# Kernel optimization log

Hardware: AMD Instinct MI355X
Metric: run time of the kernel (lower is better)

The kernel has to match this reference:

```python
import jax, jax.numpy as jnp
import numpy as np

N_NODES = 100000
N_EDGES = 1200000
D = 64            # in_channels == hidden_channels
N_GRAPHS = 512
N_CLASSES = 10
N_LAYERS = 3
BN_EPS = 1e-5


def setup_inputs() -> dict:
    key = jax.random.key(0)
    ks = jax.random.split(key, 16)
    x = jax.random.normal(ks[0], (N_NODES, D), dtype=jnp.float32)
    edge_index = jax.random.randint(ks[1], (2, N_EDGES), 0, N_NODES, dtype=jnp.int64)
    batch = jnp.sort(jax.random.randint(ks[2], (N_NODES,), 0, N_GRAPHS, dtype=jnp.int64))
    s = 1.0 / np.sqrt(D)
    # all GIN layers share shape since in_channels == hidden_channels
    mlp_w1 = jax.random.uniform(ks[3], (N_LAYERS, D, D), jnp.float32, -s, s)
    mlp_b1 = jax.random.uniform(ks[4], (N_LAYERS, D), jnp.float32, -s, s)
    mlp_w2 = jax.random.uniform(ks[5], (N_LAYERS, D, D), jnp.float32, -s, s)
    mlp_b2 = jax.random.uniform(ks[6], (N_LAYERS, D), jnp.float32, -s, s)
    bn_g = jnp.ones((N_LAYERS, D), jnp.float32)
    bn_b = jnp.zeros((N_LAYERS, D), jnp.float32)
    hw1 = jax.random.uniform(ks[7], (D, D), jnp.float32, -s, s)
    hb1 = jax.random.uniform(ks[8], (D,), jnp.float32, -s, s)
    hg1 = jnp.ones((D,), jnp.float32)
    hbb1 = jnp.zeros((D,), jnp.float32)
    hw2 = jax.random.uniform(ks[9], (D, D // 2), jnp.float32, -s, s)
    hb2 = jax.random.uniform(ks[10], (D // 2,), jnp.float32, -s, s)
    hg2 = jnp.ones((D // 2,), jnp.float32)
    hbb2 = jnp.zeros((D // 2,), jnp.float32)
    s2 = 1.0 / np.sqrt(D // 2)
    ow = jax.random.uniform(ks[11], (D // 2, N_CLASSES), jnp.float32, -s2, s2)
    ob = jax.random.uniform(ks[12], (N_CLASSES,), jnp.float32, -s2, s2)
    return dict(x=x, edge_index=edge_index, batch=batch,
                mlp_w1=mlp_w1, mlp_b1=mlp_b1, mlp_w2=mlp_w2, mlp_b2=mlp_b2,
                bn_g=bn_g, bn_b=bn_b,
                hw1=hw1, hb1=hb1, hg1=hg1, hbb1=hbb1,
                hw2=hw2, hb2=hb2, hg2=hg2, hbb2=hbb2, ow=ow, ob=ob)


def _bn(x, g, b):
    # training-mode BatchNorm1d: biased variance over the batch (node/graph) dim
    mu = jnp.mean(x, axis=0)
    var = jnp.mean((x - mu) ** 2, axis=0)
    return g * (x - mu) * jax.lax.rsqrt(var + BN_EPS) + b


def reference(x, edge_index, batch, mlp_w1, mlp_b1, mlp_w2, mlp_b2, bn_g, bn_b,
              hw1, hb1, hg1, hbb1, hw2, hb2, hg2, hbb2, ow, ob):
    src, dst = edge_index[0], edge_index[1]
    h = x
    for l in range(N_LAYERS):
        # GINConv (eps=0): h_i <- MLP(h_i + sum_{j in N(i)} h_j)
        agg = jax.ops.segment_sum(h[src], dst, num_segments=N_NODES)
        z = h + agg
        z = jax.nn.relu(z @ mlp_w1[l] + mlp_b1[l]) @ mlp_w2[l] + mlp_b2[l]
        h = jax.nn.relu(_bn(z, bn_g[l], bn_b[l]))
        # dropout omitted (deterministic eval)
    # global mean pool per graph
    sums = jax.ops.segment_sum(h, batch, num_segments=N_GRAPHS)
    cnts = jax.ops.segment_sum(jnp.ones((N_NODES,), h.dtype), batch, num_segments=N_GRAPHS)
    g = sums / jnp.maximum(cnts, 1.0)[:, None]
    g = jax.nn.relu(_bn(g @ hw1 + hb1, hg1, hbb1))
    g = jax.nn.relu(_bn(g @ hw2 + hb2, hg2, hbb2))
    return g @ ow + ob
```

## Files before the change

### kernel.cpp

```cpp
#include <hip/hip_runtime.h>
#include <hip/hip_bf16.h>

#define N_NODES 100000
#define N_EDGES 1200000
#define NG 512

typedef float f32;
typedef unsigned short u16;
typedef unsigned short us8 __attribute__((ext_vector_type(8)));
typedef __bf16 bf16x8 __attribute__((ext_vector_type(8)));
typedef float f32x16 __attribute__((ext_vector_type(16)));

__device__ __forceinline__ f32 bf2f(u16 v) {
  return __uint_as_float(((unsigned)v) << 16);
}
__device__ __forceinline__ u16 f2bf(f32 f) {
  __hip_bfloat16 b = __float2bfloat16(f);
  return *reinterpret_cast<u16*>(&b);
}

__global__ void k_detect(const int* __restrict__ w, int* __restrict__ flag) {
  int t = threadIdx.x;
  int acc = 0;
  #pragma unroll
  for (int k = 0; k < 8; ++k) acc |= w[(t * 8 + k) * 2 + 1];
  if (acc) atomicOr(flag, 1);
}

__global__ void k_count(const int* __restrict__ w, const int* __restrict__ flag,
                        int* __restrict__ deg, int* __restrict__ rank) {
  int e = blockIdx.x * 256 + threadIdx.x;
  if (e >= N_EDGES) return;
  int d = flag[0] ? w[N_EDGES + e] : w[2 * (N_EDGES + e)];
  rank[e] = atomicAdd(&deg[d], 1);
}

__global__ void k_scan1(const int* __restrict__ deg, int* __restrict__ incl, int* __restrict__ bsums) {
  __shared__ int sd[256];
  int t = threadIdx.x, b = blockIdx.x;
  int base = b * 1024 + t * 4;
  int v0 = (base + 0 < N_NODES) ? deg[base + 0] : 0;
  int v1 = (base + 1 < N_NODES) ? deg[base + 1] : 0;
  int v2 = (base + 2 < N_NODES) ? deg[base + 2] : 0;
  int v3 = (base + 3 < N_NODES) ? deg[base + 3] : 0;
  int s = v0 + v1 + v2 + v3;
  sd[t] = s; __syncthreads();
  for (int off = 1; off < 256; off <<= 1) {
    int x = (t >= off) ? sd[t - off] : 0; __syncthreads();
    sd[t] += x; __syncthreads();
  }
  int run = sd[t] - s;
  run += v0; if (base + 0 < N_NODES) incl[base + 0] = run;
  run += v1; if (base + 1 < N_NODES) incl[base + 1] = run;
  run += v2; if (base + 2 < N_NODES) incl[base + 2] = run;
  run += v3; if (base + 3 < N_NODES) incl[base + 3] = run;
  if (t == 255) bsums[b] = sd[255];
}

__global__ void k_scan2(int* __restrict__ bsums, int nb) {
  __shared__ int sd[128];
  int t = threadIdx.x;
  int v = (t < nb) ? bsums[t] : 0;
  sd[t] = v; __syncthreads();
  for (int off = 1; off < 128; off <<= 1) {
    int x = (t >= off) ? sd[t - off] : 0; __syncthreads();
    sd[t] += x; __syncthreads();
  }
  if (t < nb) bsums[t] = sd[t] - v;
}

__global__ void k_scan3(const int* __restrict__ incl, const int* __restrict__ bsums,
                        int* __restrict__ offs) {
  int i = blockIdx.x * 256 + threadIdx.x;
  if (i >= N_NODES) return;
  int start = (i == 0) ? 0 : (incl[i - 1] + bsums[(i - 1) >> 10]);
  offs[i] = start;
  if (i == N_NODES - 1) offs[N_NODES] = incl[i] + bsums[i >> 10];
}

__global__ void k_fill(const int* __restrict__ w, const int* __restrict__ flag,
                       const int* __restrict__ offs, const int* __restrict__ rank,
                       int* __restrict__ csr) {
  int e = blockIdx.x * 256 + threadIdx.x;
  if (e >= N_EDGES) return;
  int is32 = flag[0];
  int s = is32 ? w[e] : w[2 * e];
  int d = is32 ? w[N_EDGES + e] : w[2 * (N_EDGES + e)];
  csr[offs[d] + rank[e]] = s;
}

__global__ void k_cast(const f32* __restrict__ x, u16* __restrict__ h) {
  int i = blockIdx.x * 256 + threadIdx.x;
  if (i >= N_NODES * 8) return;
  float4 v0 = ((const float4*)x)[i * 2 + 0];
  float4 v1 = ((const float4*)x)[i * 2 + 1];
  us8 r;
  r[0] = f2bf(v0.x); r[1] = f2bf(v0.y); r[2] = f2bf(v0.z); r[3] = f2bf(v0.w);
  r[4] = f2bf(v1.x); r[5] = f2bf(v1.y); r[6] = f2bf(v1.z); r[7] = f2bf(v1.w);
  *(us8*)&h[i * 8] = r;
}

__global__ __launch_bounds__(256) void k_agg(const u16* __restrict__ hin,
                                             u16* __restrict__ z,
                                             const int* __restrict__ offs,
                                             const int* __restrict__ csr) {
  int wid = blockIdx.x * 4 + (threadIdx.x >> 6);
  int lane = threadIdx.x & 63;
  int slot = lane >> 3;
  int fl = (lane & 7) << 3;
  int e0 = offs[wid], e1 = offs[wid + 1];
  f32 a0[8] = {0,0,0,0,0,0,0,0};
  f32 a1[8] = {0,0,0,0,0,0,0,0};
  int e = e0 + slot;
  for (; e + 8 < e1; e += 16) {
    int s0 = csr[e], s1 = csr[e + 8];
    us8 v0 = *(const us8*)&hin[s0 * 64 + fl];
    us8 v1 = *(const us8*)&hin[s1 * 64 + fl];
    #pragma unroll
    for (int k = 0; k < 8; ++k) { a0[k] += bf2f(v0[k]); a1[k] += bf2f(v1[k]); }
  }
  if (e < e1) {
    us8 v0 = *(const us8*)&hin[csr[e] * 64 + fl];
    #pragma unroll
    for (int k = 0; k < 8; ++k) a0[k] += bf2f(v0[k]);
  }
  #pragma unroll
  for (int k = 0; k < 8; ++k) a0[k] += a1[k];
  #pragma unroll
  for (int k = 0; k < 8; ++k) {
    a0[k] += __shfl_xor(a0[k], 8);
    a0[k] += __shfl_xor(a0[k], 16);
    a0[k] += __shfl_xor(a0[k], 32);
  }
  if (slot == 0) {
    us8 sv = *(const us8*)&hin[wid * 64 + fl];
    us8 o;
    #pragma unroll
    for (int k = 0; k < 8; ++k) o[k] = f2bf(a0[k] + bf2f(sv[k]));
    *(us8*)&z[wid * 64 + fl] = o;
  }
}

__global__ __launch_bounds__(256) void k_mlp(
    const u16* __restrict__ zin, f32* __restrict__ yout,
    const f32* __restrict__ W1, const f32* __restrict__ b1,
    const f32* __restrict__ W2, const f32* __restrict__ b2,
    f32* __restrict__ stsum, f32* __restrict__ stsq)
{
  __shared__ __align__(16) u16 zs[128 * 64];
  __shared__ __align__(16) u16 wt1[64 * 64];
  __shared__ __align__(16) u16 wt2[64 * 64];
  __shared__ __align__(16) u16 mid[4 * 32 * 64];
  __shared__ f32 b1s[64], b2s[64], blks[64], blkq[64];
  const int t = threadIdx.x;
  char* zb = (char*)zs; char* w1b = (char*)wt1; char* w2b = (char*)wt2; char* mb = (char*)mid;
  const int base = blockIdx.x * 128;
  #pragma unroll
  for (int r = 0; r < 4; ++r) {
    int off = r * 4096 + t * 16;
    int row = off >> 7, c = off & 127;
    *(us8*)(zb + row * 128 + (c ^ ((row & 7) << 4))) =
        *(const us8*)((const char*)(zin + (size_t)base * 64) + off);
  }
  #pragma unroll
  for (int i0 = 0; i0 < 16; ++i0) {
    int i = i0 * 256 + t;
    int k = i >> 6, c = i & 63;
    int off = c * 128 + ((k * 2) ^ ((c & 7) << 4));
    *(u16*)(w1b + off) = f2bf(W1[i]);
    *(u16*)(w2b + off) = f2bf(W2[i]);
  }
  if (t < 64) { b1s[t] = b1[t]; b2s[t] = b2[t]; blks[t] = 0.f; blkq[t] = 0.f; }
  __syncthreads();
  const int wv = t >> 6, l = t & 63;
  const int lr = l & 31, lh = l >> 5;
  f32x16 acc0, acc1;
  #pragma unroll
  for (int i = 0; i < 16; ++i) { acc0[i] = 0.f; acc1[i] = 0.f; }
  #pragma unroll
  for (int s = 0; s < 4; ++s) {
    int kb = s * 32 + lh * 16;
    int arow = wv * 32 + lr;
    bf16x8 a  = *(bf16x8*)(zb + arow * 128 + (kb ^ ((arow & 7) << 4)));
    bf16x8 bA = *(bf16x8*)(w1b + lr * 128 + (kb ^ ((lr & 7) << 4)));
    bf16x8 bB = *(bf16x8*)(w1b + (lr + 32) * 128 + (kb ^ (((lr + 32) & 7) << 4)));
    acc0 = __builtin_amdgcn_mfma_f32_32x32x16_bf16(a, bA, acc0, 0, 0, 0);
    acc1 = __builtin_amdgcn_mfma_f32_32x32x16_bf16(a, bB, acc1, 0, 0, 0);
  }
  #pragma unroll
  for (int g = 0; g < 16; ++g) {
    int rowl = (g & 3) + 8 * (g >> 2) + 4 * lh;
    int roff = wv * 4096 + rowl * 128;
    int sw = (rowl & 7) << 4;
    *(u16*)(mb + roff + ((lr * 2) ^ sw))        = f2bf(fmaxf(acc0[g] + b1s[lr], 0.f));
    *(u16*)(mb + roff + (((lr + 32) * 2) ^ sw)) = f2bf(fmaxf(acc1[g] + b1s[lr + 32], 0.f));
  }
  asm volatile("s_waitcnt lgkmcnt(0)" ::: "memory");
  #pragma unroll
  for (int i = 0; i < 16; ++i) { acc0[i] = 0.f; acc1[i] = 0.f; }
  #pragma unroll
  for (int s = 0; s < 4; ++s) {
    int kb = s * 32 + lh * 16;
    bf16x8 a  = *(bf16x8*)(mb + wv * 4096 + lr * 128 + (kb ^ ((lr & 7) << 4)));
    bf16x8 bA = *(bf16x8*)(w2b + lr * 128 + (kb ^ ((lr & 7) << 4)));
    bf16x8 bB = *(bf16x8*)(w2b + (lr + 32) * 128 + (kb ^ (((lr + 32) & 7) << 4)));
    acc0 = __builtin_amdgcn_mfma_f32_32x32x16_bf16(a, bA, acc0, 0, 0, 0);
    acc1 = __builtin_amdgcn_mfma_f32_32x32x16_bf16(a, bB, acc1, 0, 0, 0);
  }
  f32 ps0 = 0, pq0 = 0, ps1 = 0, pq1 = 0;
  #pragma unroll
  for (int g = 0; g < 16; ++g) {
    int rowl = (g & 3) + 8 * (g >> 2) + 4 * lh;
    int node = base + wv * 32 + rowl;
    if (node < N_NODES) {
      f32 y0 = acc0[g] + b2s[lr];
      f32 y1 = acc1[g] + b2s[lr + 32];
      yout[(size_t)node * 64 + lr] = y0;
      yout[(size_t)node * 64 + lr + 32] = y1;
      ps0 += y0; pq0 += y0 * y0;
      ps1 += y1; pq1 += y1 * y1;
    }
  }
  atomicAdd(&blks[lr], ps0);      atomicAdd(&blkq[lr], pq0);
  atomicAdd(&blks[lr + 32], ps1); atomicAdd(&blkq[lr + 32], pq1);
  __syncthreads();
  if (t < 64) { atomicAdd(&stsum[t], blks[t]); atomicAdd(&stsq[t], blkq[t]); }
}

__global__ void k_hfin(const f32* __restrict__ st, const f32* __restrict__ g,
                       const f32* __restrict__ b, f32* __restrict__ ss, f32 invn, int d) {
  int t = threadIdx.x;
  if (t < d) {
    f32 m = st[t] * invn;
    f32 var = st[64 + t] * invn - m * m;
    f32 inv = rsqrtf(var + 1e-5f);
    f32 sc = g[t] * inv;
    ss[t] = sc;
    ss[64 + t] = b[t] - m * sc;
  }
}

__global__ void k_bnapply(const f32* __restrict__ y, u16* __restrict__ h,
                          const f32* __restrict__ ss) {
  int i = blockIdx.x * 256 + threadIdx.x;
  if (i >= N_NODES * 8) return;
  int c0 = (i & 7) * 8;
  float4 v0 = ((const float4*)y)[i * 2 + 0];
  float4 v1 = ((const float4*)y)[i * 2 + 1];
  us8 r;
  r[0] = f2bf(fmaxf(fmaf(v0.x, ss[c0 + 0], ss[64 + c0 + 0]), 0.f));
  r[1] = f2bf(fmaxf(fmaf(v0.y, ss[c0 + 1], ss[64 + c0 + 1]), 0.f));
  r[2] = f2bf(fmaxf(fmaf(v0.z, ss[c0 + 2], ss[64 + c0 + 2]), 0.f));
  r[3] = f2bf(fmaxf(fmaf(v0.w, ss[c0 + 3], ss[64 + c0 + 3]), 0.f));
  r[4] = f2bf(fmaxf(fmaf(v1.x, ss[c0 + 4], ss[64 + c0 + 4]), 0.f));
  r[5] = f2bf(fmaxf(fmaf(v1.y, ss[c0 + 5], ss[64 + c0 + 5]), 0.f));
  r[6] = f2bf(fmaxf(fmaf(v1.z, ss[c0 + 6], ss[64 + c0 + 6]), 0.f));
  r[7] = f2bf(fmaxf(fmaf(v1.w, ss[c0 + 7], ss[64 + c0 + 7]), 0.f));
  *(us8*)&h[i * 8] = r;
}

__global__ void k_pool(const u16* __restrict__ h, const int* __restrict__ bw,
                       const int* __restrict__ flag,
                       f32* __restrict__ gsum, f32* __restrict__ gcnt) {
  int wid = (blockIdx.x * blockDim.x + threadIdx.x) >> 6;
  int lane = threadIdx.x & 63;
  const int nw = (256 * 256) >> 6;
  const int per = (N_NODES + nw - 1) / nw;
  int s = wid * per; int e = s + per; if (e > N_NODES) e = N_NODES;
  if (s >= e) return;
  int is32 = flag[0];
  int g = is32 ? bw[s] : bw[2 * s];
  f32 acc = 0.f, cnt = 0.f;
  for (int i = s; i < e; ++i) {
    int gi = is32 ? bw[i] : bw[2 * i];
    if (gi != g) {
      atomicAdd(&gsum[g * 64 + lane], acc);
      if (lane == 0) atomicAdd(&gcnt[g], cnt);
      g = gi; acc = 0.f; cnt = 0.f;
    }
    acc += bf2f(h[i * 64 + lane]);
    cnt += 1.f;
  }
  atomicAdd(&gsum[g * 64 + lane], acc);
  if (lane == 0) atomicAdd(&gcnt[g], cnt);
}

__global__ __launch_bounds__(256) void k_head1(const f32* __restrict__ gsum, const f32* __restrict__ gcnt,
                                               const f32* __restrict__ W, const f32* __restrict__ bias,
                                               f32* __restrict__ p, f32* __restrict__ st) {
  __shared__ f32 Ws[4096];
  __shared__ f32 zs[4][64];
  __shared__ f32 bs[64], bq[64];
  int t = threadIdx.x;
  for (int i = t; i < 4096; i += 256) Ws[i] = W[i];
  if (t < 64) { bs[t] = 0.f; bq[t] = 0.f; }
  int wave = t >> 6, lane = t & 63;
  int row = blockIdx.x * 4 + wave;
  f32 z = gsum[row * 64 + lane] / fmaxf(gcnt[row], 1.f);
  zs[wave][lane] = z;
  __syncthreads();
  f32 y = bias[lane];
  for (int f = 0; f < 64; ++f) y = fmaf(zs[wave][f], Ws[f * 64 + lane], y);
  p[row * 64 + lane] = y;
  atomicAdd(&bs[lane], y);
  atomicAdd(&bq[lane], y * y);
  __syncthreads();
  if (t < 64) { atomicAdd(&st[t], bs[t]); atomicAdd(&st[64 + t], bq[t]); }
}

__global__ __launch_bounds__(256) void k_head2(const f32* __restrict__ p1, const f32* __restrict__ ss,
                                               const f32* __restrict__ W, const f32* __restrict__ bias,
                                               f32* __restrict__ p2, f32* __restrict__ st) {
  __shared__ f32 Ws[2048];
  __shared__ f32 zs[4][64];
  __shared__ f32 bs[32], bq[32];
  int t = threadIdx.x;
  for (int i = t; i < 2048; i += 256) Ws[i] = W[i];
  if (t < 32) { bs[t] = 0.f; bq[t] = 0.f; }
  int wave = t >> 6, lane = t & 63;
  int row = blockIdx.x * 4 + wave;
  f32 z = fmaxf(fmaf(p1[row * 64 + lane], ss[lane], ss[64 + lane]), 0.f);
  zs[wave][lane] = z;
  __syncthreads();
  if (lane < 32) {
    f32 y = bias[lane];
    for (int f = 0; f < 64; ++f) y = fmaf(zs[wave][f], Ws[f * 32 + lane], y);
    p2[row * 32 + lane] = y;
    atomicAdd(&bs[lane], y);
    atomicAdd(&bq[lane], y * y);
  }
  __syncthreads();
  if (t < 32) { atomicAdd(&st[t], bs[t]); atomicAdd(&st[64 + t], bq[t]); }
}

__global__ __launch_bounds__(256) void k_head3(const f32* __restrict__ p2, const f32* __restrict__ ss,
                                               const f32* __restrict__ W, const f32* __restrict__ bias,
                                               f32* __restrict__ out) {
  __shared__ f32 Ws[320];
  __shared__ f32 obs[10];
  __shared__ f32 zs[4][32];
  int t = threadIdx.x;
  for (int i = t; i < 320; i += 256) Ws[i] = W[i];
  if (t < 10) obs[t] = bias[t];
  int wave = t >> 6, lane = t & 63;
  int row = blockIdx.x * 4 + wave;
  if (lane < 32) zs[wave][lane] = fmaxf(fmaf(p2[row * 32 + lane], ss[lane], ss[64 + lane]), 0.f);
  __syncthreads();
  if (lane < 10) {
    f32 o = obs[lane];
    for (int f = 0; f < 32; ++f) o = fmaf(zs[wave][f], Ws[f * 10 + lane], o);
    out[row * 10 + lane] = o;
  }
}

extern "C" void kernel_launch(void* const* d_in, const int* in_sizes, int n_in,
                              void* d_out, int out_size, void* d_ws, size_t ws_size,
                              hipStream_t stream) {
  (void)in_sizes; (void)n_in; (void)out_size; (void)ws_size;
  const f32* x    = (const f32*)d_in[0];
  const int* eiw  = (const int*)d_in[1];
  const int* btw  = (const int*)d_in[2];
  const f32* mw1  = (const f32*)d_in[3];
  const f32* mb1  = (const f32*)d_in[4];
  const f32* mw2  = (const f32*)d_in[5];
  const f32* mb2  = (const f32*)d_in[6];
  const f32* bng  = (const f32*)d_in[7];
  const f32* bnb  = (const f32*)d_in[8];
  const f32* hw1  = (const f32*)d_in[9];
  const f32* hb1  = (const f32*)d_in[10];
  const f32* hg1  = (const f32*)d_in[11];
  const f32* hbb1 = (const f32*)d_in[12];
  const f32* hw2  = (const f32*)d_in[13];
  const f32* hb2  = (const f32*)d_in[14];
  const f32* hg2  = (const f32*)d_in[15];
  const f32* hbb2 = (const f32*)d_in[16];
  const f32* ow   = (const f32*)d_in[17];
  const f32* ob   = (const f32*)d_in[18];
  f32* out = (f32*)d_out;

  int* deg    = (int*)d_ws;
  int* incl   = deg + N_NODES;
  int* bsums  = incl + N_NODES;
  int* flag   = bsums + 128;
  int* offs   = flag + 4;
  int* rank   = offs + 100004;
  int* csr    = rank + N_EDGES;
  u16* hbuf   = (u16*)(csr + N_EDGES);
  u16* zbuf   = hbuf + (size_t)N_NODES * 64;
  f32* ybuf   = (f32*)(zbuf + (size_t)100096 * 64);
  f32* stats  = ybuf + (size_t)N_NODES * 64;
  f32* ss     = stats + 1024;
  f32* ss2    = ss + 128;
  f32* gsum   = ss2 + 128;
  f32* gcnt   = gsum + NG * 64;
  f32* p1     = gcnt + NG;
  f32* p2     = p1 + NG * 64;

  hipMemsetAsync(deg, 0, N_NODES * sizeof(int), stream);
  hipMemsetAsync(flag, 0, sizeof(int), stream);
  hipMemsetAsync(stats, 0, 1024 * sizeof(f32), stream);
  hipMemsetAsync(gsum, 0, (NG * 64 + NG) * sizeof(f32), stream);

  k_detect<<<1, 256, 0, stream>>>(eiw, flag);
  k_count<<<(N_EDGES + 255) / 256, 256, 0, stream>>>(eiw, flag, deg, rank);
  k_scan1<<<(N_NODES + 1023) / 1024, 256, 0, stream>>>(deg, incl, bsums);
  k_scan2<<<1, 128, 0, stream>>>(bsums, (N_NODES + 1023) / 1024);
  k_scan3<<<(N_NODES + 255) / 256, 256, 0, stream>>>(incl, bsums, offs);
  k_fill<<<(N_EDGES + 255) / 256, 256, 0, stream>>>(eiw, flag, offs, rank, csr);

  const int AGG_GRID = N_NODES / 4;
  const int MLP_GRID = (N_NODES + 127) / 128;
  const int C8_GRID  = (N_NODES * 8 + 255) / 256;

  k_cast<<<C8_GRID, 256, 0, stream>>>(x, hbuf);
  k_agg<<<AGG_GRID, 256, 0, stream>>>(hbuf, zbuf, offs, csr);
  k_mlp<<<MLP_GRID, 256, 0, stream>>>(zbuf, ybuf, mw1,        mb1,       mw2,        mb2,       stats + 0,   stats + 64);
  k_hfin<<<1, 64, 0, stream>>>(stats + 0, bng + 0, bnb + 0, ss, 1.f / N_NODES, 64);
  k_bnapply<<<C8_GRID, 256, 0, stream>>>(ybuf, hbuf, ss);
  k_agg<<<AGG_GRID, 256, 0, stream>>>(hbuf, zbuf, offs, csr);
  k_mlp<<<MLP_GRID, 256, 0, stream>>>(zbuf, ybuf, mw1 + 4096, mb1 + 64,  mw2 + 4096, mb2 + 64,  stats + 128, stats + 192);
  k_hfin<<<1, 64, 0, stream>>>(stats + 128, bng + 64, bnb + 64, ss, 1.f / N_NODES, 64);
  k_bnapply<<<C8_GRID, 256, 0, stream>>>(ybuf, hbuf, ss);
  k_agg<<<AGG_GRID, 256, 0, stream>>>(hbuf, zbuf, offs, csr);
  k_mlp<<<MLP_GRID, 256, 0, stream>>>(zbuf, ybuf, mw1 + 8192, mb1 + 128, mw2 + 8192, mb2 + 128, stats + 256, stats + 320);
  k_hfin<<<1, 64, 0, stream>>>(stats + 256, bng + 128, bnb + 128, ss, 1.f / N_NODES, 64);
  k_bnapply<<<C8_GRID, 256, 0, stream>>>(ybuf, hbuf, ss);

  k_pool<<<256, 256, 0, stream>>>(hbuf, btw, flag, gsum, gcnt);
  k_head1<<<NG / 4, 256, 0, stream>>>(gsum, gcnt, hw1, hb1, p1, stats + 384);
  k_hfin<<<1, 64, 0, stream>>>(stats + 384, hg1, hbb1, ss, 1.f / NG, 64);
  k_head2<<<NG / 4, 256, 0, stream>>>(p1, ss, hw2, hb2, p2, stats + 512);
  k_hfin<<<1, 64, 0, stream>>>(stats + 512, hg2, hbb2, ss2, 1.f / NG, 32);
  k_head3<<<NG / 4, 256, 0, stream>>>(p2, ss2, ow, ob, out);
}
```

Before: 521.8 us.

## Fuse BN finalize into consumers, stage MLP output via LDS, vectorize CSR build

Removes the separate k_hfin launches by computing BatchNorm scale/shift inside each consumer kernel. The last layer's BN apply is folded into the pooling kernel, which now reads the fp32 pre-BN output directly. The MLP epilogue stages results through LDS so global stores become coalesced float4 writes. Count and fill process two edges per thread with vector loads, and the four memsets are merged into one. Every block now recomputes the stats, and pooling reads fp32 instead of bf16 data.

```diff
diff --git a/kernel.cpp b/kernel.cpp
--- a/kernel.cpp
+++ b/kernel.cpp
@@ -29,10 +29,20 @@
 
 __global__ void k_count(const int* __restrict__ w, const int* __restrict__ flag,
                         int* __restrict__ deg, int* __restrict__ rank) {
-  int e = blockIdx.x * 256 + threadIdx.x;
-  if (e >= N_EDGES) return;
-  int d = flag[0] ? w[N_EDGES + e] : w[2 * (N_EDGES + e)];
-  rank[e] = atomicAdd(&deg[d], 1);
+  int e2 = blockIdx.x * 256 + threadIdx.x;
+  if (e2 >= N_EDGES / 2) return;
+  int d0, d1;
+  if (flag[0]) {
+    int2 dd = *(const int2*)&w[N_EDGES + 2 * e2];
+    d0 = dd.x; d1 = dd.y;
+  } else {
+    int4 dd = *(const int4*)&w[2 * N_EDGES + 4 * e2];
+    d0 = dd.x; d1 = dd.z;
+  }
+  int2 rk;
+  rk.x = atomicAdd(&deg[d0], 1);
+  rk.y = atomicAdd(&deg[d1], 1);
+  *(int2*)&rank[2 * e2] = rk;
 }
 
 __global__ void k_scan1(const int* __restrict__ deg, int* __restrict__ incl, int* __restrict__ bsums) {
@@ -81,12 +91,21 @@
 __global__ void k_fill(const int* __restrict__ w, const int* __restrict__ flag,
                        const int* __restrict__ offs, const int* __restrict__ rank,
                        int* __restrict__ csr) {
-  int e = blockIdx.x * 256 + threadIdx.x;
-  if (e >= N_EDGES) return;
-  int is32 = flag[0];
-  int s = is32 ? w[e] : w[2 * e];
-  int d = is32 ? w[N_EDGES + e] : w[2 * (N_EDGES + e)];
-  csr[offs[d] + rank[e]] = s;
+  int e2 = blockIdx.x * 256 + threadIdx.x;
+  if (e2 >= N_EDGES / 2) return;
+  int s0, s1, d0, d1;
+  if (flag[0]) {
+    int2 sv = *(const int2*)&w[2 * e2];
+    int2 dv = *(const int2*)&w[N_EDGES + 2 * e2];
+    s0 = sv.x; s1 = sv.y; d0 = dv.x; d1 = dv.y;
+  } else {
+    int4 sv = *(const int4*)&w[4 * e2];
+    int4 dv = *(const int4*)&w[2 * N_EDGES + 4 * e2];
+    s0 = sv.x; s1 = sv.z; d0 = dv.x; d1 = dv.z;
+  }
+  int2 rk = *(const int2*)&rank[2 * e2];
+  csr[offs[d0] + rk.x] = s0;
+  csr[offs[d1] + rk.y] = s1;
 }
 
 __global__ void k_cast(const f32* __restrict__ x, u16* __restrict__ h) {
@@ -147,13 +166,16 @@
     const f32* __restrict__ W2, const f32* __restrict__ b2,
     f32* __restrict__ stsum, f32* __restrict__ stsq)
 {
-  __shared__ __align__(16) u16 zs[128 * 64];
-  __shared__ __align__(16) u16 wt1[64 * 64];
-  __shared__ __align__(16) u16 wt2[64 * 64];
-  __shared__ __align__(16) u16 mid[4 * 32 * 64];
-  __shared__ f32 b1s[64], b2s[64], blks[64], blkq[64];
+  __shared__ __align__(16) char lds[50176];
+  char* zb  = lds;
+  char* w1b = lds + 16384;
+  char* w2b = lds + 24576;
+  char* mb  = lds + 32768;
+  f32* b1s  = (f32*)(lds + 49152);
+  f32* b2s  = b1s + 64;
+  f32* blks = b2s + 64;
+  f32* blkq = blks + 64;
   const int t = threadIdx.x;
-  char* zb = (char*)zs; char* w1b = (char*)wt1; char* w2b = (char*)wt2; char* mb = (char*)mid;
   const int base = blockIdx.x * 128;
   #pragma unroll
   for (int r = 0; r < 4; ++r) {
@@ -207,42 +229,50 @@
     acc0 = __builtin_amdgcn_mfma_f32_32x32x16_bf16(a, bA, acc0, 0, 0, 0);
     acc1 = __builtin_amdgcn_mfma_f32_32x32x16_bf16(a, bB, acc1, 0, 0, 0);
   }
+  __syncthreads();
+  char* yb = lds + wv * 8192;
   f32 ps0 = 0, pq0 = 0, ps1 = 0, pq1 = 0;
   #pragma unroll
   for (int g = 0; g < 16; ++g) {
     int rowl = (g & 3) + 8 * (g >> 2) + 4 * lh;
-    int node = base + wv * 32 + rowl;
-    if (node < N_NODES) {
-      f32 y0 = acc0[g] + b2s[lr];
-      f32 y1 = acc1[g] + b2s[lr + 32];
-      yout[(size_t)node * 64 + lr] = y0;
-      yout[(size_t)node * 64 + lr + 32] = y1;
+    f32 y0 = acc0[g] + b2s[lr];
+    f32 y1 = acc1[g] + b2s[lr + 32];
+    *(f32*)(yb + rowl * 256 + lr * 4)        = y0;
+    *(f32*)(yb + rowl * 256 + (lr + 32) * 4) = y1;
+    if (base + wv * 32 + rowl < N_NODES) {
       ps0 += y0; pq0 += y0 * y0;
       ps1 += y1; pq1 += y1 * y1;
     }
   }
+  asm volatile("s_waitcnt lgkmcnt(0)" ::: "memory");
+  __builtin_amdgcn_sched_barrier(0);
+  #pragma unroll
+  for (int k = 0; k < 8; ++k) {
+    int row = k * 4 + (l >> 4);
+    float4 v = *(float4*)(yb + row * 256 + (l & 15) * 16);
+    int node = base + wv * 32 + row;
+    if (node < N_NODES)
+      *(float4*)&yout[(size_t)node * 64 + (l & 15) * 4] = v;
+  }
   atomicAdd(&blks[lr], ps0);      atomicAdd(&blkq[lr], pq0);
   atomicAdd(&blks[lr + 32], ps1); atomicAdd(&blkq[lr + 32], pq1);
   __syncthreads();
   if (t < 64) { atomicAdd(&stsum[t], blks[t]); atomicAdd(&stsq[t], blkq[t]); }
 }
 
-__global__ void k_hfin(const f32* __restrict__ st, const f32* __restrict__ g,
-                       const f32* __restrict__ b, f32* __restrict__ ss, f32 invn, int d) {
-  int t = threadIdx.x;
-  if (t < d) {
-    f32 m = st[t] * invn;
-    f32 var = st[64 + t] * invn - m * m;
-    f32 inv = rsqrtf(var + 1e-5f);
-    f32 sc = g[t] * inv;
-    ss[t] = sc;
-    ss[64 + t] = b[t] - m * sc;
-  }
-}
-
-__global__ void k_bnapply(const f32* __restrict__ y, u16* __restrict__ h,
-                          const f32* __restrict__ ss) {
-  int i = blockIdx.x * 256 + threadIdx.x;
+__global__ __launch_bounds__(256) void k_bnfin(const f32* __restrict__ y, u16* __restrict__ h,
+                                               const f32* __restrict__ st,
+                                               const f32* __restrict__ g, const f32* __restrict__ b) {
+  __shared__ f32 ss[128];
+  int t = threadIdx.x;
+  if (t < 64) {
+    f32 m = st[t] * (1.f / N_NODES);
+    f32 var = st[64 + t] * (1.f / N_NODES) - m * m;
+    f32 sc = g[t] * rsqrtf(var + 1e-5f);
+    ss[t] = sc; ss[64 + t] = b[t] - m * sc;
+  }
+  __syncthreads();
+  int i = blockIdx.x * 256 + t;
   if (i >= N_NODES * 8) return;
   int c0 = (i & 7) * 8;
   float4 v0 = ((const float4*)y)[i * 2 + 0];
@@ -259,30 +289,41 @@
   *(us8*)&h[i * 8] = r;
 }
 
-__global__ void k_pool(const u16* __restrict__ h, const int* __restrict__ bw,
-                       const int* __restrict__ flag,
+__global__ void k_pool(const f32* __restrict__ y, const int* __restrict__ bw,
+                       const int* __restrict__ flag, const f32* __restrict__ st,
+                       const f32* __restrict__ g, const f32* __restrict__ b,
                        f32* __restrict__ gsum, f32* __restrict__ gcnt) {
-  int wid = (blockIdx.x * blockDim.x + threadIdx.x) >> 6;
-  int lane = threadIdx.x & 63;
+  __shared__ f32 ss[128];
+  int t = threadIdx.x;
+  if (t < 64) {
+    f32 m = st[t] * (1.f / N_NODES);
+    f32 var = st[64 + t] * (1.f / N_NODES) - m * m;
+    f32 sc = g[t] * rsqrtf(var + 1e-5f);
+    ss[t] = sc; ss[64 + t] = b[t] - m * sc;
+  }
+  __syncthreads();
+  int wid = (blockIdx.x * blockDim.x + t) >> 6;
+  int lane = t & 63;
   const int nw = (256 * 256) >> 6;
   const int per = (N_NODES + nw - 1) / nw;
   int s = wid * per; int e = s + per; if (e > N_NODES) e = N_NODES;
   if (s >= e) return;
+  f32 sc = ss[lane], sh = ss[64 + lane];
   int is32 = flag[0];
-  int g = is32 ? bw[s] : bw[2 * s];
+  int gcur = is32 ? bw[s] : bw[2 * s];
   f32 acc = 0.f, cnt = 0.f;
   for (int i = s; i < e; ++i) {
     int gi = is32 ? bw[i] : bw[2 * i];
-    if (gi != g) {
-      atomicAdd(&gsum[g * 64 + lane], acc);
-      if (lane == 0) atomicAdd(&gcnt[g], cnt);
-      g = gi; acc = 0.f; cnt = 0.f;
+    if (gi != gcur) {
+      atomicAdd(&gsum[gcur * 64 + lane], acc);
+      if (lane == 0) atomicAdd(&gcnt[gcur], cnt);
+      gcur = gi; acc = 0.f; cnt = 0.f;
     }
-    acc += bf2f(h[i * 64 + lane]);
+    acc += fmaxf(fmaf(y[(size_t)i * 64 + lane], sc, sh), 0.f);
     cnt += 1.f;
   }
-  atomicAdd(&gsum[g * 64 + lane], acc);
-  if (lane == 0) atomicAdd(&gcnt[g], cnt);
+  atomicAdd(&gsum[gcur * 64 + lane], acc);
+  if (lane == 0) atomicAdd(&gcnt[gcur], cnt);
 }
 
 __global__ __launch_bounds__(256) void k_head1(const f32* __restrict__ gsum, const f32* __restrict__ gcnt,
@@ -308,15 +349,24 @@
   if (t < 64) { atomicAdd(&st[t], bs[t]); atomicAdd(&st[64 + t], bq[t]); }
 }
 
-__global__ __launch_bounds__(256) void k_head2(const f32* __restrict__ p1, const f32* __restrict__ ss,
+__global__ __launch_bounds__(256) void k_head2(const f32* __restrict__ p1, const f32* __restrict__ st,
+                                               const f32* __restrict__ g, const f32* __restrict__ b,
                                                const f32* __restrict__ W, const f32* __restrict__ bias,
-                                               f32* __restrict__ p2, f32* __restrict__ st) {
+                                               f32* __restrict__ p2, f32* __restrict__ st2) {
   __shared__ f32 Ws[2048];
   __shared__ f32 zs[4][64];
   __shared__ f32 bs[32], bq[32];
+  __shared__ f32 ss[128];
   int t = threadIdx.x;
   for (int i = t; i < 2048; i += 256) Ws[i] = W[i];
+  if (t < 64) {
+    f32 m = st[t] * (1.f / NG);
+    f32 var = st[64 + t] * (1.f / NG) - m * m;
+    f32 sc = g[t] * rsqrtf(var + 1e-5f);
+    ss[t] = sc; ss[64 + t] = b[t] - m * sc;
+  }
   if (t < 32) { bs[t] = 0.f; bq[t] = 0.f; }
+  __syncthreads();
   int wave = t >> 6, lane = t & 63;
   int row = blockIdx.x * 4 + wave;
   f32 z = fmaxf(fmaf(p1[row * 64 + lane], ss[lane], ss[64 + lane]), 0.f);
@@ -330,21 +380,30 @@
     atomicAdd(&bq[lane], y * y);
   }
   __syncthreads();
-  if (t < 32) { atomicAdd(&st[t], bs[t]); atomicAdd(&st[64 + t], bq[t]); }
-}
-
-__global__ __launch_bounds__(256) void k_head3(const f32* __restrict__ p2, const f32* __restrict__ ss,
+  if (t < 32) { atomicAdd(&st2[t], bs[t]); atomicAdd(&st2[64 + t], bq[t]); }
+}
+
+__global__ __launch_bounds__(256) void k_head3(const f32* __restrict__ p2, const f32* __restrict__ st2,
+                                               const f32* __restrict__ g, const f32* __restrict__ b,
                                                const f32* __restrict__ W, const f32* __restrict__ bias,
                                                f32* __restrict__ out) {
   __shared__ f32 Ws[320];
   __shared__ f32 obs[10];
   __shared__ f32 zs[4][32];
+  __shared__ f32 ss[64];
   int t = threadIdx.x;
   for (int i = t; i < 320; i += 256) Ws[i] = W[i];
   if (t < 10) obs[t] = bias[t];
+  if (t < 32) {
+    f32 m = st2[t] * (1.f / NG);
+    f32 var = st2[64 + t] * (1.f / NG) - m * m;
+    f32 sc = g[t] * rsqrtf(var + 1e-5f);
+    ss[t] = sc; ss[32 + t] = b[t] - m * sc;
+  }
+  __syncthreads();
   int wave = t >> 6, lane = t & 63;
   int row = blockIdx.x * 4 + wave;
-  if (lane < 32) zs[wave][lane] = fmaxf(fmaf(p2[row * 32 + lane], ss[lane], ss[64 + lane]), 0.f);
+  if (lane < 32) zs[wave][lane] = fmaxf(fmaf(p2[row * 32 + lane], ss[lane], ss[32 + lane]), 0.f);
   __syncthreads();
   if (lane < 10) {
     f32 o = obs[lane];
@@ -378,35 +437,31 @@
   const f32* ob   = (const f32*)d_in[18];
   f32* out = (f32*)d_out;
 
-  int* deg    = (int*)d_ws;
-  int* incl   = deg + N_NODES;
-  int* bsums  = incl + N_NODES;
-  int* flag   = bsums + 128;
-  int* offs   = flag + 4;
-  int* rank   = offs + 100004;
-  int* csr    = rank + N_EDGES;
-  u16* hbuf   = (u16*)(csr + N_EDGES);
-  u16* zbuf   = hbuf + (size_t)N_NODES * 64;
-  f32* ybuf   = (f32*)(zbuf + (size_t)100096 * 64);
-  f32* stats  = ybuf + (size_t)N_NODES * 64;
-  f32* ss     = stats + 1024;
-  f32* ss2    = ss + 128;
-  f32* gsum   = ss2 + 128;
-  f32* gcnt   = gsum + NG * 64;
-  f32* p1     = gcnt + NG;
-  f32* p2     = p1 + NG * 64;
-
-  hipMemsetAsync(deg, 0, N_NODES * sizeof(int), stream);
-  hipMemsetAsync(flag, 0, sizeof(int), stream);
-  hipMemsetAsync(stats, 0, 1024 * sizeof(f32), stream);
-  hipMemsetAsync(gsum, 0, (NG * 64 + NG) * sizeof(f32), stream);
+  int* deg   = (int*)d_ws;
+  int* flag  = deg + 100000;
+  f32* stats = (f32*)(flag + 32);
+  f32* gsum  = stats + 1024;
+  f32* gcnt  = gsum + NG * 64;
+  const size_t ZERO_INTS = 100000 + 32 + 1024 + 32768 + 512;
+  int* incl  = (int*)(gcnt + NG);
+  int* bsums = incl + 100000;
+  int* offs  = bsums + 128;
+  int* rank  = offs + 100004;
+  int* csr   = rank + N_EDGES;
+  u16* hbuf  = (u16*)(csr + N_EDGES);
+  u16* zbuf  = hbuf + (size_t)N_NODES * 64;
+  f32* ybuf  = (f32*)(zbuf + (size_t)100096 * 64);
+  f32* p1    = ybuf + (size_t)N_NODES * 64;
+  f32* p2    = p1 + NG * 64;
+
+  hipMemsetAsync(deg, 0, ZERO_INTS * sizeof(int), stream);
 
   k_detect<<<1, 256, 0, stream>>>(eiw, flag);
-  k_count<<<(N_EDGES + 255) / 256, 256, 0, stream>>>(eiw, flag, deg, rank);
+  k_count<<<(N_EDGES / 2 + 255) / 256, 256, 0, stream>>>(eiw, flag, deg, rank);
   k_scan1<<<(N_NODES + 1023) / 1024, 256, 0, stream>>>(deg, incl, bsums);
   k_scan2<<<1, 128, 0, stream>>>(bsums, (N_NODES + 1023) / 1024);
   k_scan3<<<(N_NODES + 255) / 256, 256, 0, stream>>>(incl, bsums, offs);
-  k_fill<<<(N_EDGES + 255) / 256, 256, 0, stream>>>(eiw, flag, offs, rank, csr);
+  k_fill<<<(N_EDGES / 2 + 255) / 256, 256, 0, stream>>>(eiw, flag, offs, rank, csr);
 
   const int AGG_GRID = N_NODES / 4;
   const int MLP_GRID = (N_NODES + 127) / 128;
@@ -414,22 +469,16 @@
 
   k_cast<<<C8_GRID, 256, 0, stream>>>(x, hbuf);
   k_agg<<<AGG_GRID, 256, 0, stream>>>(hbuf, zbuf, offs, csr);
-  k_mlp<<<MLP_GRID, 256, 0, stream>>>(zbuf, ybuf, mw1,        mb1,       mw2,        mb2,       stats + 0,   stats + 64);
-  k_hfin<<<1, 64, 0, stream>>>(stats + 0, bng + 0, bnb + 0, ss, 1.f / N_NODES, 64);
-  k_bnapply<<<C8_GRID, 256, 0, stream>>>(ybuf, hbuf, ss);
+  k_mlp<<<MLP_GRID, 256, 0, stream>>>(zbuf, ybuf, mw1, mb1, mw2, mb2, stats + 0, stats + 64);
+  k_bnfin<<<C8_GRID, 256, 0, stream>>>(ybuf, hbuf, stats + 0, bng + 0, bnb + 0);
   k_agg<<<AGG_GRID, 256, 0, stream>>>(hbuf, zbuf, offs, csr);
-  k_mlp<<<MLP_GRID, 256, 0, stream>>>(zbuf, ybuf, mw1 + 4096, mb1 + 64,  mw2 + 4096, mb2 + 64,  stats + 128, stats + 192);
-  k_hfin<<<1, 64, 0, stream>>>(stats + 128, bng + 64, bnb + 64, ss, 1.f / N_NODES, 64);
-  k_bnapply<<<C8_GRID, 256, 0, stream>>>(ybuf, hbuf, ss);
+  k_mlp<<<MLP_GRID, 256, 0, stream>>>(zbuf, ybuf, mw1 + 4096, mb1 + 64, mw2 + 4096, mb2 + 64, stats + 128, stats + 192);
+  k_bnfin<<<C8_GRID, 256, 0, stream>>>(ybuf, hbuf, stats + 128, bng + 64, bnb + 64);
   k_agg<<<AGG_GRID, 256, 0, stream>>>(hbuf, zbuf, offs, csr);
   k_mlp<<<MLP_GRID, 256, 0, stream>>>(zbuf, ybuf, mw1 + 8192, mb1 + 128, mw2 + 8192, mb2 + 128, stats + 256, stats + 320);
-  k_hfin<<<1, 64, 0, stream>>>(stats + 256, bng + 128, bnb + 128, ss, 1.f / N_NODES, 64);
-  k_bnapply<<<C8_GRID, 256, 0, stream>>>(ybuf, hbuf, ss);
-
-  k_pool<<<256, 256, 0, stream>>>(hbuf, btw, flag, gsum, gcnt);
+
+  k_pool<<<256, 256, 0, stream>>>(ybuf, btw, flag, stats + 256, bng + 128, bnb + 128, gsum, gcnt);
   k_head1<<<NG / 4, 256, 0, stream>>>(gsum, gcnt, hw1, hb1, p1, stats + 384);
-  k_hfin<<<1, 64, 0, stream>>>(stats + 384, hg1, hbb1, ss, 1.f / NG, 64);
-  k_head2<<<NG / 4, 256, 0, stream>>>(p1, ss, hw2, hb2, p2, stats + 512);
-  k_hfin<<<1, 64, 0, stream>>>(stats + 512, hg2, hbb2, ss2, 1.f / NG, 32);
-  k_head3<<<NG / 4, 256, 0, stream>>>(p2, ss2, ow, ob, out);
-}
+  k_head2<<<NG / 4, 256, 0, stream>>>(p1, stats + 384, hg1, hbb1, hw2, hb2, p2, stats + 512);
+  k_head3<<<NG / 4, 256, 0, stream>>>(p2, stats + 512, hg2, hbb2, ow, ob, out);
+}
```

Result: faster. 486.2 us (-6.8%).
